# Kernel tuning notes

Hardware: AMD Instinct MI355X
Metric: run time of the kernel (lower is better)

Reference implementation:

```python
import jax, jax.numpy as jnp
import numpy as np

BLOCK_SIZE = 32
TAU = 0.1
E2M1_VALUES = np.array([0.0, 0.5, 1.0, 1.5, 2.0, 3.0, 4.0, 6.0], dtype=np.float32)
E2M1_BOUNDS = np.array([0.25, 0.75, 1.25, 1.75, 2.5, 3.5, 5.0], dtype=np.float32)


def setup_inputs() -> dict:
    key = jax.random.key(0)
    x = jax.random.normal(key, (2048, 4096), dtype=jnp.float32)
    return {
        "x": x,
        "delta_raw": jnp.zeros((), dtype=jnp.float32),
        "bounds_base": jnp.asarray(E2M1_BOUNDS),
        "values_table": jnp.asarray(E2M1_VALUES),
    }


def reference(x, delta_raw, bounds_base, values_table):
    orig_shape = x.shape
    bs = BLOCK_SIZE
    xb = x.reshape(-1, bs)  # [n_blocks, bs]
    # per-block e8m0 power-of-two scale from amax
    amax = jnp.max(jnp.abs(xb), axis=-1, keepdims=True)
    descale = amax / 6.0
    e8m0_scale = jnp.ceil(jnp.maximum(jnp.log2(descale), -127.0))
    scale_factor = jnp.exp2(e8m0_scale)
    x_scaled = (xb / scale_factor).reshape(orig_shape)
    # perturbed decision bounds
    shifted_bounds = bounds_base + 0.5 * jnp.tanh(delta_raw)  # [7]
    x_abs = jnp.abs(x_scaled)
    # hard ordinal bucketize: count bounds exceeded -> code in [0,7]
    ord_hard = jnp.sum(x_abs[..., None] > shifted_bounds, axis=-1)  # int32
    sign_bit = (x_scaled < 0).astype(jnp.uint8)
    codes = (sign_bit << 3) | ord_hard.astype(jnp.uint8)
    # soft ordinal weights via sigmoid at each boundary
    p = jax.nn.sigmoid((x_abs[..., None] - shifted_bounds) / TAU)  # [..., 7]
    w0 = 1.0 - p[..., 0]
    mids = p[..., :-1] - p[..., 1:]
    w_last = p[..., -1]
    weights = jnp.concatenate([w0[..., None], mids, w_last[..., None]], axis=-1)  # [..., 8]
    weights = jnp.clip(weights, 0.0)
    weights = weights / (jnp.sum(weights, axis=-1, keepdims=True) + 1e-8)
    abs_soft = jnp.sum(weights * values_table, axis=-1)
    abs_hard = values_table[ord_hard]
    # straight-through: hard value forward, soft gradient
    abs_mix = abs_soft + jax.lax.stop_gradient(abs_hard - abs_soft)
    y_scaled = jnp.where(x_scaled >= 0, abs_mix, -abs_mix)
    y = (y_scaled.reshape(-1, bs) * scale_factor).reshape(orig_shape)
    scales = (e8m0_scale + 127.0).astype(jnp.uint8)[:, 0].reshape(
        *orig_shape[:-1], orig_shape[-1] // bs
    )
    return (y, codes, scales, shifted_bounds, weights)
```

## Files before the change

kernel.cpp:

```cpp
#include <hip/hip_runtime.h>

#define BLK 256
#define EPT 4
#define WLDS (BLK * EPT * 8)

__global__ __launch_bounds__(BLK) void fp4_kernel(
    const float* __restrict__ x,
    const float* __restrict__ delta_raw,
    const float* __restrict__ bounds_base,
    const float* __restrict__ values_table,
    float* __restrict__ out, long long N)
{
    const int tid = threadIdx.x;
    const long long base = (long long)blockIdx.x * (BLK * EPT);
    const long long g0 = base + (long long)(tid * EPT);

    __shared__ float s_vals[8];
    __shared__ __align__(16) float s_w[WLDS];

    if (tid < 8) s_vals[tid] = values_table[tid];

    const float ht = 0.5f * tanhf(delta_raw[0]);
    const float C = 14.426950408889634f;
    float sb[7], cb[7];
#pragma unroll
    for (int j = 0; j < 7; ++j) { sb[j] = bounds_base[j] + ht; cb[j] = sb[j] * C; }
    float vt[8];
#pragma unroll
    for (int k = 0; k < 8; ++k) vt[k] = values_table[k];

    __syncthreads();

    const float4 xv = *reinterpret_cast<const float4*>(x + g0);
    const float xe[EPT] = {xv.x, xv.y, xv.z, xv.w};

    float a = fmaxf(fmaxf(fabsf(xe[0]), fabsf(xe[1])),
                    fmaxf(fabsf(xe[2]), fabsf(xe[3])));
    a = fmaxf(a, __shfl_xor(a, 1));
    a = fmaxf(a, __shfl_xor(a, 2));
    a = fmaxf(a, __shfl_xor(a, 4));

    const float descale = a / 6.0f;
    const float e = ceilf(fmaxf(log2f(descale), -127.0f));
    const int ie = (int)e;
    const float inv_scale = __int_as_float((127 - ie) << 23);
    const float scale = (ie == -127) ? __int_as_float(0x00400000)
                                     : __int_as_float((ie + 127) << 23);

    const int wkey = (tid & 7) << 2;
    float ys[EPT], cd[EPT];

#pragma unroll
    for (int i = 0; i < EPT; ++i) {
        const float xs = xe[i] * inv_scale;
        const float xa = fabsf(xs);

        int ord = 0;
#pragma unroll
        for (int j = 0; j < 7; ++j) ord += (xa > sb[j]) ? 1 : 0;

        const float xac = xa * C;
        float p[7];
#pragma unroll
        for (int j = 0; j < 7; ++j) {
            const float ex = exp2f(cb[j] - xac);
            p[j] = __builtin_amdgcn_rcpf(1.0f + ex);
        }

        float w[8];
        w[0] = 1.0f - p[0];
#pragma unroll
        for (int j = 1; j < 7; ++j) w[j] = p[j - 1] - p[j];
        w[7] = p[6];

        float sum = 0.0f;
#pragma unroll
        for (int k = 0; k < 8; ++k) { w[k] = fmaxf(w[k], 0.0f); sum += w[k]; }
        const float inv = __builtin_amdgcn_rcpf(sum + 1e-8f);

        float abs_soft = 0.0f;
#pragma unroll
        for (int k = 0; k < 8; ++k) { w[k] *= inv; abs_soft += w[k] * vt[k]; }

        const float abs_hard = s_vals[ord];
        const float abs_mix = abs_soft + (abs_hard - abs_soft);
        ys[i] = ((xs >= 0.0f) ? abs_mix : -abs_mix) * scale;
        cd[i] = (float)(((xs < 0.0f) ? 8 : 0) | ord);

        const int f = (tid * EPT + i) * 8;
        *reinterpret_cast<float4*>(&s_w[(f + 0) ^ wkey]) =
            make_float4(w[0], w[1], w[2], w[3]);
        *reinterpret_cast<float4*>(&s_w[(f + 4) ^ wkey]) =
            make_float4(w[4], w[5], w[6], w[7]);
    }

    *reinterpret_cast<float4*>(out + g0)     = make_float4(ys[0], ys[1], ys[2], ys[3]);
    *reinterpret_cast<float4*>(out + N + g0) = make_float4(cd[0], cd[1], cd[2], cd[3]);
    if ((tid & 7) == 0) out[2 * N + (g0 >> 5)] = e + 127.0f;
    if (blockIdx.x == 0 && tid < 7) out[2 * N + (N >> 5) + tid] = sb[tid];

    __syncthreads();

    const long long wbase = 2 * N + (N >> 5) + 7 + (long long)blockIdx.x * WLDS;
    const int rbase = tid ^ (((tid >> 5) & 7) << 2);
#pragma unroll
    for (int k = 0; k < 32; ++k) {
        out[wbase + tid + (k << 8)] = s_w[rbase + (k << 8)];
    }
}

extern "C" void kernel_launch(void* const* d_in, const int* in_sizes, int n_in,
                              void* d_out, int out_size, void* d_ws, size_t ws_size,
                              hipStream_t stream) {
    const float* x      = (const float*)d_in[0];
    const float* delta  = (const float*)d_in[1];
    const float* bounds = (const float*)d_in[2];
    const float* vals   = (const float*)d_in[3];
    float* out = (float*)d_out;
    const long long N = (long long)in_sizes[0];
    const int nblocks = (int)(N / (BLK * EPT));
    fp4_kernel<<<nblocks, BLK, 0, stream>>>(x, delta, bounds, vals, out, N);
}
```

Baseline: 358.3 us.

## Vectorize weight stores by shifting LDS layout to align global float4 writes

Rearranges the shared-memory weight staging so each element's 8 weights are offset by one float. The unaligned global weight region can then be written with 16-byte float4 stores instead of 32 scalar stores per thread, with a special wraparound for the final quad. It also halves elements per thread, widens the amax shuffle reduction to 16 lanes, and raises the occupancy hint. The alignment trick assumes the weight-region base offset is 3 mod 4 floats, which holds for this shape.

```diff
diff --git a/kernel.cpp b/kernel.cpp
--- a/kernel.cpp
+++ b/kernel.cpp
@@ -1,10 +1,14 @@
 #include <hip/hip_runtime.h>
 
 #define BLK 256
-#define EPT 4
-#define WLDS (BLK * EPT * 8)
+#define EPT 2
+#define ELEMS (BLK * EPT)
+#define WFLOATS (ELEMS * 8)
 
-__global__ __launch_bounds__(BLK) void fp4_kernel(
+__device__ __forceinline__ int swz_q(int q) { return q ^ ((q >> 4) & 7); }
+__device__ __forceinline__ int swz(int p)  { return (swz_q(p >> 2) << 2) | (p & 3); }
+
+__global__ __launch_bounds__(BLK, 8) void fp4_kernel(
     const float* __restrict__ x,
     const float* __restrict__ delta_raw,
     const float* __restrict__ bounds_base,
@@ -12,15 +16,16 @@
     float* __restrict__ out, long long N)
 {
     const int tid = threadIdx.x;
-    const long long base = (long long)blockIdx.x * (BLK * EPT);
-    const long long g0 = base + (long long)(tid * EPT);
+    const long long base = (long long)blockIdx.x * ELEMS;
+    const long long g0 = base + 2 * tid;
 
     __shared__ float s_vals[8];
-    __shared__ __align__(16) float s_w[WLDS];
+    __shared__ __align__(16) float s_w[WFLOATS];
 
     if (tid < 8) s_vals[tid] = values_table[tid];
 
-    const float ht = 0.5f * tanhf(delta_raw[0]);
+    float ht = 0.5f * tanhf(delta_raw[0]);
+    ht = __int_as_float(__builtin_amdgcn_readfirstlane(__float_as_int(ht)));
     const float C = 14.426950408889634f;
     float sb[7], cb[7];
 #pragma unroll
@@ -31,14 +36,14 @@
 
     __syncthreads();
 
-    const float4 xv = *reinterpret_cast<const float4*>(x + g0);
-    const float xe[EPT] = {xv.x, xv.y, xv.z, xv.w};
+    const float2 xv = *reinterpret_cast<const float2*>(x + g0);
+    const float xe[EPT] = {xv.x, xv.y};
 
-    float a = fmaxf(fmaxf(fabsf(xe[0]), fabsf(xe[1])),
-                    fmaxf(fabsf(xe[2]), fabsf(xe[3])));
+    float a = fmaxf(fabsf(xe[0]), fabsf(xe[1]));
     a = fmaxf(a, __shfl_xor(a, 1));
     a = fmaxf(a, __shfl_xor(a, 2));
     a = fmaxf(a, __shfl_xor(a, 4));
+    a = fmaxf(a, __shfl_xor(a, 8));
 
     const float descale = a / 6.0f;
     const float e = ceilf(fmaxf(log2f(descale), -127.0f));
@@ -47,7 +52,6 @@
     const float scale = (ie == -127) ? __int_as_float(0x00400000)
                                      : __int_as_float((ie + 127) << 23);
 
-    const int wkey = (tid & 7) << 2;
     float ys[EPT], cd[EPT];
 
 #pragma unroll
@@ -87,25 +91,40 @@
         ys[i] = ((xs >= 0.0f) ? abs_mix : -abs_mix) * scale;
         cd[i] = (float)(((xs < 0.0f) ? 8 : 0) | ord);
 
-        const int f = (tid * EPT + i) * 8;
-        *reinterpret_cast<float4*>(&s_w[(f + 0) ^ wkey]) =
-            make_float4(w[0], w[1], w[2], w[3]);
-        *reinterpret_cast<float4*>(&s_w[(f + 4) ^ wkey]) =
-            make_float4(w[4], w[5], w[6], w[7]);
+        const int el = 2 * tid + i;
+        s_w[swz(((el << 3) - 1) & (WFLOATS - 1))] = w[0];
+        *reinterpret_cast<float4*>(&s_w[swz_q(el << 1) << 2]) =
+            make_float4(w[1], w[2], w[3], w[4]);
+        const int qb = swz_q((el << 1) | 1) << 2;
+        *reinterpret_cast<float2*>(&s_w[qb]) = make_float2(w[5], w[6]);
+        s_w[qb + 2] = w[7];
     }
 
-    *reinterpret_cast<float4*>(out + g0)     = make_float4(ys[0], ys[1], ys[2], ys[3]);
-    *reinterpret_cast<float4*>(out + N + g0) = make_float4(cd[0], cd[1], cd[2], cd[3]);
-    if ((tid & 7) == 0) out[2 * N + (g0 >> 5)] = e + 127.0f;
-    if (blockIdx.x == 0 && tid < 7) out[2 * N + (N >> 5) + tid] = sb[tid];
+    *reinterpret_cast<float2*>(out + g0)     = make_float2(ys[0], ys[1]);
+    *reinterpret_cast<float2*>(out + N + g0) = make_float2(cd[0], cd[1]);
+    if ((tid & 15) == 0) out[2 * N + (g0 >> 5)] = e + 127.0f;
+    if (blockIdx.x == 0 && tid < 7) {
+        float v = sb[0];
+#pragma unroll
+        for (int j = 1; j < 7; ++j) v = (tid == j) ? sb[j] : v;
+        out[2 * N + (N >> 5) + tid] = v;
+    }
 
     __syncthreads();
 
-    const long long wbase = 2 * N + (N >> 5) + 7 + (long long)blockIdx.x * WLDS;
-    const int rbase = tid ^ (((tid >> 5) & 7) << 2);
+    const long long S = 2 * N + (N >> 5) + 7 + (long long)blockIdx.x * WFLOATS;
 #pragma unroll
-    for (int k = 0; k < 32; ++k) {
-        out[wbase + tid + (k << 8)] = s_w[rbase + (k << 8)];
+    for (int k = 0; k < 4; ++k) {
+        const int q = tid + (k << 8);
+        const float4 v = *reinterpret_cast<const float4*>(&s_w[swz_q(q) << 2]);
+        if (q != 1023) {
+            *reinterpret_cast<float4*>(out + (S + 1 + 4 * (long long)q)) = v;
+        } else {
+            out[S + 4093] = v.x;
+            out[S + 4094] = v.y;
+            out[S + 4095] = v.z;
+            out[S]        = v.w;
+        }
     }
 }
 
@@ -118,6 +137,6 @@
     const float* vals   = (const float*)d_in[3];
     float* out = (float*)d_out;
     const long long N = (long long)in_sizes[0];
-    const int nblocks = (int)(N / (BLK * EPT));
+    const int nblocks = (int)(N / ELEMS);
     fp4_kernel<<<nblocks, BLK, 0, stream>>>(x, delta, bounds, vals, out, N);
 }
```

Measured after the change: 359.8 us. No clear change (+0.4%).
